# Optimization experiments

Hardware: AMD Instinct MI355X
Metric: run time of the kernel (lower is better)

Reference implementation:

```python
import jax, jax.numpy as jnp
import numpy as np

N_SEQ = 512      # n: number of generation steps (rows of x_tensor)
N_POOL = 4096    # candidate node pool size (rows of f_tensor / a_tensor)
N_FEAT = 20
E = 64           # n_node_embed
G = 128          # n_graph_embed
S = 16           # n_seq_embed
ALPHA = 20       # n_seq_alphabets


def setup_inputs() -> dict:
    key = jax.random.key(0)
    ks = jax.random.split(key, 16)
    f32 = jnp.float32

    def lin(k, fan_in, shape):
        return jax.random.normal(k, shape, f32) / jnp.sqrt(jnp.asarray(fan_in, f32))

    return {
        "x_tensor": jax.random.normal(ks[0], (N_SEQ, ALPHA), f32),
        "f_tensor": jax.random.normal(ks[1], (N_POOL, N_FEAT), f32),
        "a_tensor": jax.random.uniform(ks[2], (N_POOL, N_POOL), f32),
        "d_tensor": jax.random.uniform(ks[3], (N_POOL, N_POOL), f32),
        "w_feat": lin(ks[4], N_FEAT, (N_FEAT, E)),
        "b_feat": lin(ks[5], N_FEAT, (E,)),
        "w_gcn1": lin(ks[6], E, (E, E)),   # GCN W1, bias=False
        "w_gcn2": lin(ks[7], E, (E, E)),   # GCN W1, bias=False
        "w_graph": lin(ks[8], E, (E, G)),
        "b_graph": lin(ks[9], E, (G,)),
        "w_gate": lin(ks[10], E, (E, G)),
        "b_gate": lin(ks[11], E, (G,)),
        "w_edge": lin(ks[12], 2 * E + S + G, (2 * E + S + G, 1)),
        "b_edge": lin(ks[13], 2 * E + S + G, (1,)),
        "w_seq": lin(ks[14], ALPHA, (ALPHA, S)),
        "b_seq": lin(ks[15], ALPHA, (S,)),
    }


def reference(x_tensor, f_tensor, a_tensor, d_tensor,
              w_feat, b_feat, w_gcn1, w_gcn2,
              w_graph, b_graph, w_gate, b_gate,
              w_edge, b_edge, w_seq, b_seq):
    n = x_tensor.shape[0]
    Np = f_tensor.shape[0]
    e = w_feat.shape[1]
    g_dim = w_graph.shape[1]

    seq_embed = x_tensor @ w_seq + b_seq                 # [n, S]
    f_nodes_in = f_tensor @ w_feat + b_feat              # [Np, E]
    dAd = (d_tensor @ a_tensor) @ d_tensor               # gcn1: D A D
    h_nodes_in = (dAd @ jax.nn.relu(f_nodes_in)) @ w_gcn1  # [Np, E]

    # Chain graph at step k has k+1 nodes; A = I + sub/super diagonals.
    # Degrees: 1 (k==0), 2 at endpoints, 3 interior. Dh[k, i] = deg^{-1/2}, masked.
    ii = jnp.arange(n)
    kk = ii[:, None]
    jj = ii[None, :]
    deg = jnp.where((jj == 0) | (jj == kk), 2.0, 3.0)
    deg = jnp.where(kk == 0, 1.0, deg)
    Dh = jnp.where(jj <= kk, deg ** -0.5, 0.0).astype(x_tensor.dtype)  # [n, n]

    def step(carry, k):
        mask, idxs, h_last, h_graph = carry
        z = jnp.concatenate([
            h_nodes_in,
            jnp.broadcast_to(h_last, (Np, e)),
            jnp.broadcast_to(seq_embed[k], (Np, seq_embed.shape[1])),
            jnp.broadcast_to(h_graph, (Np, g_dim)),
        ], axis=1)                                        # [Np, 2E+S+G]
        score = ((jax.nn.relu(z) * mask[:, None]) @ w_edge)[:, 0] + b_edge[0]
        idx = jnp.argmax(score)
        mask = mask.at[idx].set(0.0)
        idxs = idxs.at[k].set(idx.astype(jnp.int32))

        # gcn2 on the chain graph over the k+1 selected nodes (band-structured).
        F_sel = f_nodes_in[idxs]                          # [n, E]; rows > k masked by dh
        dh = Dh[k]                                        # [n]
        gmat = dh[:, None] * F_sel
        g_up = jnp.pad(gmat, ((0, 1), (0, 0)))[1:]        # g[i+1]
        g_dn = jnp.pad(gmat, ((1, 0), (0, 0)))[:-1]       # g[i-1]
        dF = dh[:, None] * (gmat + g_up + g_dn)           # (D A D) F on the chain
        h_nodes = dF @ w_gcn2                             # [n, E]; rows > k are zero
        h_last_new = jnp.take(h_nodes, k, axis=0)

        valid = (jnp.arange(n) <= k).astype(h_nodes.dtype)[:, None]
        hg = h_nodes @ w_graph + b_graph
        gg = h_nodes @ w_gate + b_gate
        h_graph_new = jnp.sum(hg * jax.nn.sigmoid(gg) * valid, axis=0)
        return (mask, idxs, h_last_new, h_graph_new), score

    init = (jnp.ones(Np, x_tensor.dtype),
            jnp.zeros(n, jnp.int32),
            jnp.zeros(e, x_tensor.dtype),
            jnp.zeros(g_dim, x_tensor.dtype))
    (_, idxs, _, _), scores = jax.lax.scan(step, init, jnp.arange(n))
    return scores, idxs
```

## Files before the change

kernel.cpp:

```cpp
#include <hip/hip_runtime.h>
#include <math.h>

#define NPOOL 4096
#define NSEQ  512
#define NF    20
#define EDIM  64
#define GDIM  128
#define SDIM  16
#define ALPH  20
#define SPLITK 16
#define KSLICE (NPOOL / SPLITK)

__device__ __forceinline__ double relu_d(double x){ return x > 0.0 ? x : 0.0; }
__device__ __forceinline__ double sigm_d(double x){ return 1.0 / (1.0 + exp(-x)); }

__device__ __forceinline__ unsigned long long sortable_u64(double x) {
    x = x + 0.0;
    unsigned long long b = (unsigned long long)__double_as_longlong(x);
    return b ^ ((b >> 63) ? ~0ULL : 0x8000000000000000ULL);
}

__global__ __launch_bounds__(256) void k_prep(const float* __restrict__ f, const float* __restrict__ wf,
                       const float* __restrict__ bf, double* __restrict__ Fin, double* __restrict__ R,
                       double* __restrict__ T1z) {
    int t = blockIdx.x * 256 + threadIdx.x;
    int i = t >> 6, e = t & 63;
    double acc = (double)bf[e];
#pragma unroll
    for (int j = 0; j < NF; ++j)
        acc += (double)f[i * NF + j] * (double)wf[j * EDIM + e];
    Fin[t] = acc;
    R[t] = acc > 0.0 ? acc : 0.0;
    T1z[t] = 0.0;
}

__global__ __launch_bounds__(256) void k_seqe(const float* __restrict__ x, const float* __restrict__ wsq,
                       const float* __restrict__ bsq, double* __restrict__ seqe, int* __restrict__ rank) {
    int t = blockIdx.x * 256 + threadIdx.x;
    int k = t >> 4, s = t & 15;
    double acc = (double)bsq[s];
#pragma unroll
    for (int q = 0; q < ALPH; ++q)
        acc += (double)x[k * ALPH + q] * (double)wsq[q * SDIM + s];
    seqe[t] = acc;
    if (t < NPOOL) rank[t] = 1 << 30;
}

__global__ __launch_bounds__(256) void k_zero(double* __restrict__ buf) {
    buf[(size_t)blockIdx.x * 256 + threadIdx.x] = 0.0;
}

__global__ __launch_bounds__(256, 4) void gemm_f64_v3(const float* __restrict__ A, const double* __restrict__ B,
                                                      double* __restrict__ C) {
    __shared__ double As[32][66];
    __shared__ double Bs[32][66];
    int t  = threadIdx.x;
    int tx = t & 15;
    int ty = t >> 4;
    int row0 = blockIdx.x * 64;
    int k0   = blockIdx.y * KSLICE;
    double acc[4][4] = {};
    for (int kt = k0; kt < k0 + KSLICE; kt += 32) {
        {
            int r = t >> 2, kq = t & 3;
            const float* Ap = A + (size_t)(row0 + r) * NPOOL + kt + kq * 8;
            float4 f0 = *(const float4*)Ap;
            float4 f1 = *(const float4*)(Ap + 4);
            int kb = kq * 8;
            As[kb + 0][r] = (double)f0.x; As[kb + 1][r] = (double)f0.y;
            As[kb + 2][r] = (double)f0.z; As[kb + 3][r] = (double)f0.w;
            As[kb + 4][r] = (double)f1.x; As[kb + 5][r] = (double)f1.y;
            As[kb + 6][r] = (double)f1.z; As[kb + 7][r] = (double)f1.w;
        }
#pragma unroll
        for (int it = 0; it < 8; ++it) {
            int l = t + 256 * it;
            int kr = l >> 6, cc = l & 63;
            Bs[kr][cc] = B[(size_t)(kt + kr) * 64 + cc];
        }
        __syncthreads();
#pragma unroll
        for (int kk = 0; kk < 32; ++kk) {
            double2 a01 = *(const double2*)&As[kk][2 * ty];
            double2 a23 = *(const double2*)&As[kk][2 * ty + 32];
            double2 b01 = *(const double2*)&Bs[kk][2 * tx];
            double2 b23 = *(const double2*)&Bs[kk][2 * tx + 32];
            double a[4] = {a01.x, a01.y, a23.x, a23.y};
            double b[4] = {b01.x, b01.y, b23.x, b23.y};
#pragma unroll
            for (int i = 0; i < 4; ++i)
#pragma unroll
                for (int j = 0; j < 4; ++j)
                    acc[i][j] = fma(a[i], b[j], acc[i][j]);
        }
        __syncthreads();
    }
    int rr[4] = {2 * ty, 2 * ty + 1, 2 * ty + 32, 2 * ty + 33};
    int cc[4] = {2 * tx, 2 * tx + 1, 2 * tx + 32, 2 * tx + 33};
#pragma unroll
    for (int i = 0; i < 4; ++i)
#pragma unroll
        for (int j = 0; j < 4; ++j)
            unsafeAtomicAdd(&C[(size_t)(row0 + rr[i]) * 64 + cc[j]], acc[i][j]);
}

__global__ __launch_bounds__(256) void k_head(const double* __restrict__ T3, const float* __restrict__ w1,
                       const float* __restrict__ we, double* __restrict__ s) {
    __shared__ float w1s[64 * 64];
    int tt = threadIdx.x;
    for (int i = tt; i < 64 * 64; i += 256) w1s[i] = w1[i];
    __syncthreads();
    int row = (blockIdx.x * 256 + tt) >> 6;
    int e = tt & 63;
    const double* r = T3 + (size_t)row * 64;
    double h = 0.0;
#pragma unroll
    for (int c = 0; c < 64; ++c)
        h += r[c] * (double)w1s[c * 64 + e];
    double p = (h > 0.0 ? h : 0.0) * (double)we[e];
    for (int off = 32; off; off >>= 1) p += __shfl_down(p, off, 64);
    if (e == 0) s[row] = p;
}

__global__ __launch_bounds__(1024) void k_sort3(const double* __restrict__ s, int* __restrict__ order,
                        double* __restrict__ skey, int* __restrict__ orderB) {
    __shared__ unsigned long long P[NPOOL];
    __shared__ int idxF[NPOOL];
    __shared__ int fbS;
    int t = threadIdx.x;
    if (t == 0) fbS = 0;
    unsigned long long v[4];
#pragma unroll
    for (int i = 0; i < 4; ++i) {
        int e = 4 * t + i;
        unsigned long long srt = sortable_u64(s[e]);
        v[i] = ((~(srt >> 12)) << 12) | (unsigned long long)e;
    }

#define SHFL_ROUND(jj, kk)                                                        \
    {                                                                             \
        int lm = (int)((jj) >> 2);                                                \
        _Pragma("unroll")                                                         \
        for (int i = 0; i < 4; ++i) {                                             \
            unsigned long long p = (unsigned long long)__shfl_xor((long long)v[i], lm, 64); \
            unsigned e = 4u * (unsigned)t + (unsigned)i;                          \
            bool takeMin = (((e & (jj)) == 0u) == ((e & (kk)) == 0u));            \
            unsigned long long mn = v[i] < p ? v[i] : p;                          \
            unsigned long long mx = v[i] < p ? p : v[i];                          \
            v[i] = takeMin ? mn : mx;                                             \
        }                                                                         \
    }

#define LOCAL_ROUNDS(kk)                                                          \
    {                                                                             \
        if ((kk) >= 4) {                                                          \
            _Pragma("unroll")                                                     \
            for (int i = 0; i < 2; ++i) {                                         \
                unsigned e = 4u * (unsigned)t + (unsigned)i;                      \
                bool asc = ((e & (kk)) == 0u);                                    \
                unsigned long long a = v[i], b = v[i + 2];                        \
                bool sw = asc ? (a > b) : (a < b);                                \
                v[i] = sw ? b : a; v[i + 2] = sw ? a : b;                         \
            }                                                                     \
        }                                                                         \
        _Pragma("unroll")                                                         \
        for (int i = 0; i < 4; i += 2) {                                          \
            unsigned e = 4u * (unsigned)t + (unsigned)i;                          \
            bool asc = ((e & (kk)) == 0u);                                        \
            unsigned long long a = v[i], b = v[i + 1];                            \
            bool sw = asc ? (a > b) : (a < b);                                    \
            v[i] = sw ? b : a; v[i + 1] = sw ? a : b;                             \
        }                                                                         \
    }

    for (unsigned k = 2; k <= 256; k <<= 1) {
        for (unsigned j = k >> 1; j >= 4; j >>= 1) SHFL_ROUND(j, k)
        LOCAL_ROUNDS(k)
    }
    for (unsigned k = 512; k <= 4096; k <<= 1) {
        for (unsigned j = k >> 1; j >= 256; j >>= 1) {
            __syncthreads();
            P[4 * t + 0] = v[0]; P[4 * t + 1] = v[1];
            P[4 * t + 2] = v[2]; P[4 * t + 3] = v[3];
            __syncthreads();
            unsigned base = (4u * (unsigned)t) ^ j;
#pragma unroll
            for (int i = 0; i < 4; ++i) {
                unsigned e = 4u * (unsigned)t + (unsigned)i;
                unsigned long long p = P[base + i];
                bool takeMin = (((e & j) == 0u) == ((e & k) == 0u));
                unsigned long long mn = v[i] < p ? v[i] : p;
                unsigned long long mx = v[i] < p ? p : v[i];
                v[i] = takeMin ? mn : mx;
            }
        }
        for (unsigned j = 128; j >= 4; j >>= 1) SHFL_ROUND(j, k)
        LOCAL_ROUNDS(k)
    }
#undef SHFL_ROUND
#undef LOCAL_ROUNDS

    __syncthreads();
    P[4 * t + 0] = v[0]; P[4 * t + 1] = v[1];
    P[4 * t + 2] = v[2]; P[4 * t + 3] = v[3];
    __syncthreads();
    if (t < 512) {
        unsigned long long pa = P[t], pb = P[t + 1];
        if ((pa >> 12) == (pb >> 12)) {
            int ia = (int)(pa & 4095ULL), ib = (int)(pb & 4095ULL);
            if (sortable_u64(s[ia]) != sortable_u64(s[ib])) atomicOr(&fbS, 1);
        }
    }
    __syncthreads();
    if (fbS == 0) {
        if (t < NSEQ) {
            int id = (int)(P[t] & 4095ULL);
            order[t] = id; skey[t] = s[id]; orderB[t] = (int)(P[0] & 4095ULL);
        }
        return;
    }
    for (int i = t; i < NPOOL; i += 1024) { P[i] = sortable_u64(s[i]); idxF[i] = i; }
    __syncthreads();
    for (int k2 = 2; k2 <= NPOOL; k2 <<= 1) {
        for (int j = k2 >> 1; j > 0; j >>= 1) {
            for (int tt = t; tt < NPOOL; tt += 1024) {
                int l = tt ^ j;
                if (l > tt) {
                    unsigned long long ka = P[tt], kb = P[l];
                    int ia = idxF[tt], ib = idxF[l];
                    bool aBefore = (ka > kb) || (ka == kb && ia < ib);
                    bool asc = ((tt & k2) == 0);
                    if (asc ? !aBefore : aBefore) { P[tt] = kb; P[l] = ka; idxF[tt] = ib; idxF[l] = ia; }
                }
            }
            __syncthreads();
        }
    }
    for (int tt = t; tt < NSEQ; tt += 1024) {
        int id = idxF[tt];
        order[tt] = id; skey[tt] = s[id]; orderB[tt] = idxF[0];
    }
}

__global__ __launch_bounds__(256) void k_perk2(const double* __restrict__ Fin, const int* __restrict__ orderA,
                       const int* __restrict__ orderBv,
                       const float* __restrict__ w2, const float* __restrict__ wgr, const float* __restrict__ bgr,
                       const float* __restrict__ wga, const float* __restrict__ bga,
                       double* __restrict__ phi_inf, double* __restrict__ phi_pair, double* __restrict__ hlast) {
    const double r2 = 0.70710678118654752440;
    const double r3 = 0.57735026918962576451;
    __shared__ double u[4][64];
    __shared__ double comb[3][64];
    __shared__ double v[3][64];
    __shared__ double hgg[3][2][GDIM];
    int which = blockIdx.x >> 9;
    int k = blockIdx.x & (NSEQ - 1);
    const int* order = which ? orderBv : orderA;
    double* pi = phi_inf  + (size_t)which * NSEQ * GDIM;
    double* pp = phi_pair + (size_t)which * NSEQ * GDIM;
    double* hl = hlast    + (size_t)which * NSEQ * 64;
    int t = threadIdx.x;
    {
        int w = t >> 6, e = t & 63;
        int j = k - 3 + w;
        u[w][e] = (j >= 0) ? Fin[(size_t)order[j] * 64 + e] : 0.0;
    }
    __syncthreads();
    if (t < 192) {
        int w = t >> 6, e = t & 63;
        double dh_km3 = (k - 3 == 0) ? r2 : r3;
        double dh_km2 = (k - 2 == 0) ? r2 : r3;
        double dh_km1 = (k - 1 == 0) ? r2 : r3;
        double outer, c0, c1, c2, c3;
        if (w == 0) {
            outer = dh_km2; c0 = dh_km3; c1 = dh_km2; c2 = dh_km1; c3 = 0.0;
        } else if (w == 1) {
            outer = dh_km1; c0 = 0.0; c1 = dh_km2; c2 = dh_km1; c3 = r2;
        } else {
            if (k == 0) { outer = 1.0; c0 = c1 = c2 = 0.0; c3 = 1.0; }
            else        { outer = r2;  c0 = c1 = 0.0; c2 = dh_km1; c3 = r2; }
        }
        comb[w][e] = outer * (c0 * u[0][e] + c1 * u[1][e] + c2 * u[2][e] + c3 * u[3][e]);
    }
    __syncthreads();
    if (t < 192) {
        int w = t >> 6, e = t & 63;
        double acc = 0.0;
#pragma unroll
        for (int j = 0; j < 64; ++j)
            acc += comb[w][j] * (double)w2[j * 64 + e];
        v[w][e] = acc;
    }
    __syncthreads();
    for (int rep = 0; rep < 3; ++rep) {
        int d = t & 127, g = t >> 7;
        const float* W = g ? wga : wgr;
        const float* B = g ? bga : bgr;
        double acc = (double)B[d];
#pragma unroll
        for (int j = 0; j < 64; ++j)
            acc += v[rep][j] * (double)W[j * GDIM + d];
        hgg[rep][g][d] = acc;
    }
    __syncthreads();
    if (t < 128) {
        if (k >= 2) pi[(size_t)(k - 2) * GDIM + t] = hgg[0][0][t] * sigm_d(hgg[0][1][t]);
        double ppv = hgg[2][0][t] * sigm_d(hgg[2][1][t]);
        if (k >= 1) ppv += hgg[1][0][t] * sigm_d(hgg[1][1][t]);
        pp[(size_t)k * GDIM + t] = ppv;
    } else if (t < 192) {
        hl[(size_t)k * 64 + (t - 128)] = v[2][t - 128];
    }
}

__global__ __launch_bounds__(512) void k_scan2(const double* __restrict__ phi_inf, const double* __restrict__ phi_pair,
                       double* __restrict__ hgr) {
    __shared__ double sb[NSEQ];
    int which = blockIdx.x >> 7;
    int d = blockIdx.x & (GDIM - 1), t = threadIdx.x;
    const double* pi = phi_inf  + (size_t)which * NSEQ * GDIM;
    const double* pp = phi_pair + (size_t)which * NSEQ * GDIM;
    double* hg = hgr + (size_t)which * NSEQ * GDIM;
    sb[t] = (t >= 2) ? pi[(size_t)(t - 2) * GDIM + d] : 0.0;
    for (int off = 1; off < NSEQ; off <<= 1) {
        __syncthreads();
        double add = (t >= off) ? sb[t - off] : 0.0;
        __syncthreads();
        sb[t] += add;
    }
    __syncthreads();
    hg[(size_t)t * GDIM + d] = sb[t] + pp[(size_t)t * GDIM + d];
}

__global__ __launch_bounds__(64) void k_c2(const double* __restrict__ hlast, const double* __restrict__ hgr,
                   const double* __restrict__ seqe, const float* __restrict__ we,
                   double* __restrict__ cA, double* __restrict__ cB) {
    int which = blockIdx.x >> 9;
    int k = blockIdx.x & (NSEQ - 1), j = threadIdx.x;
    const double* hl = hlast + (size_t)which * NSEQ * 64;
    const double* hg = hgr   + (size_t)which * NSEQ * GDIM;
    double* c = which ? cB : cA;
    double ts = 0.0;
    if (k > 0) {
        ts += relu_d(hl[(size_t)(k - 1) * 64 + j]) * (double)we[64 + j];
        ts += relu_d(hg[(size_t)(k - 1) * GDIM + j]) * (double)we[144 + j];
        ts += relu_d(hg[(size_t)(k - 1) * GDIM + 64 + j]) * (double)we[208 + j];
    }
    if (j < 16) ts += relu_d(seqe[(size_t)k * SDIM + j]) * (double)we[128 + j];
    for (int off = 32; off; off >>= 1) ts += __shfl_down(ts, off, 64);
    if (j == 0) c[k] = ts;
}

__global__ __launch_bounds__(512) void k_verify2(const double* __restrict__ skey, const double* __restrict__ cA,
                         const double* __restrict__ cB, int* __restrict__ flagA, int* __restrict__ flagB) {
    __shared__ int bad;
    int t = threadIdx.x;
    if (t == 0) bad = 0;
    __syncthreads();
    if (blockIdx.x == 0) {
        if (t >= 1 && !(skey[t] + cA[t] > 0.0)) atomicOr(&bad, 1);
        __syncthreads();
        if (t == 0) flagA[0] = bad;
    } else {
        if (t >= 1 && (skey[1] + cB[t] > 0.0)) atomicOr(&bad, 1);
        __syncthreads();
        if (t == 0) flagB[0] = bad;
    }
}

__global__ __launch_bounds__(512) void k_select(const int* __restrict__ flagA, const int* __restrict__ flagB,
                        const double* __restrict__ cA, const double* __restrict__ cB,
                        const int* __restrict__ order, double* __restrict__ c,
                        int* __restrict__ idxs_sel, int* __restrict__ mode) {
    int t = threadIdx.x;
    if (flagA[0] == 0) {
        c[t] = cA[t]; idxs_sel[t] = order[t];
        if (t == 0) mode[0] = 0;
    } else if (flagB[0] == 0) {
        c[t] = cB[t]; idxs_sel[t] = order[0];
        if (t == 0) mode[0] = 1;
    } else {
        if (t == 0) mode[0] = 2;
    }
}

__global__ __launch_bounds__(256) void k_fallback(const int* __restrict__ mode,
        const double* __restrict__ Fin, const int* __restrict__ order, const double* __restrict__ skey,
        const double* __restrict__ seqe,
        const float* __restrict__ w2, const float* __restrict__ wgr, const float* __restrict__ bgr,
        const float* __restrict__ wga, const float* __restrict__ bga, const float* __restrict__ we,
        int* __restrict__ idxs_sel, double* __restrict__ c) {
    if (mode[0] != 2) return;
    const double r2 = 0.70710678118654752440;
    const double r3 = 0.57735026918962576451;
    __shared__ double u[4][64];
    __shared__ double comb[3][64];
    __shared__ double v[3][64];
    __shared__ double hgg[3][2][GDIM];
    __shared__ double Phi[GDIM], hgraph[GDIM], hlastS[64];
    __shared__ int selS, ptrS, minS_;
    int t = threadIdx.x;
    if (t < 64) { u[0][t] = u[1][t] = u[2][t] = u[3][t] = 0.0; hlastS[t] = 0.0; }
    if (t < 128) { Phi[t] = 0.0; hgraph[t] = 0.0; }
    if (t == 0) { ptrS = 0; minS_ = 0x7fffffff; }
    __syncthreads();
    for (int k = 0; k < NSEQ; ++k) {
        if (t < 64) {
            int j = t;
            double ts = relu_d(hlastS[j]) * (double)we[64 + j]
                      + relu_d(hgraph[j]) * (double)we[144 + j]
                      + relu_d(hgraph[64 + j]) * (double)we[208 + j];
            if (j < 16) ts += relu_d(seqe[(size_t)k * SDIM + j]) * (double)we[128 + j];
            for (int off = 32; off; off >>= 1) ts += __shfl_down(ts, off, 64);
            if (j == 0) {
                c[k] = ts;
                int ptr = ptrS, idx;
                if (ptr == 0) { idx = order[0]; minS_ = idx; ptrS = 1; }
                else if (skey[ptr] + ts > 0.0) {
                    idx = order[ptr];
                    if (idx < minS_) minS_ = idx;
                    ptrS = ptr + 1;
                } else idx = minS_;
                selS = idx;
                idxs_sel[k] = idx;
            }
        }
        __syncthreads();
        int idx = selS;
        if (t < 64) u[k & 3][t] = Fin[(size_t)idx * 64 + t];
        __syncthreads();
        if (t < 192) {
            int w = t >> 6, e = t & 63;
            double dh_km3 = (k - 3 == 0) ? r2 : r3;
            double dh_km2 = (k - 2 == 0) ? r2 : r3;
            double dh_km1 = (k - 1 == 0) ? r2 : r3;
            double outer, c0, c1, c2, c3;
            if (w == 0) {
                outer = dh_km2; c0 = dh_km3; c1 = dh_km2; c2 = dh_km1; c3 = 0.0;
            } else if (w == 1) {
                outer = dh_km1; c0 = 0.0; c1 = dh_km2; c2 = dh_km1; c3 = r2;
            } else {
                if (k == 0) { outer = 1.0; c0 = c1 = c2 = 0.0; c3 = 1.0; }
                else        { outer = r2;  c0 = c1 = 0.0; c2 = dh_km1; c3 = r2; }
            }
            double uu0 = u[(k - 3) & 3][e], uu1 = u[(k - 2) & 3][e], uu2 = u[(k - 1) & 3][e], uu3 = u[k & 3][e];
            comb[w][e] = outer * (c0 * uu0 + c1 * uu1 + c2 * uu2 + c3 * uu3);
        }
        __syncthreads();
        if (t < 192) {
            int w = t >> 6, e = t & 63;
            double acc = 0.0;
#pragma unroll
            for (int j = 0; j < 64; ++j)
                acc += comb[w][j] * (double)w2[j * 64 + e];
            v[w][e] = acc;
        }
        __syncthreads();
        for (int rep = 0; rep < 3; ++rep) {
            int d = t & 127, g = t >> 7;
            const float* W = g ? wga : wgr;
            const float* B = g ? bga : bgr;
            double acc = (double)B[d];
#pragma unroll
            for (int j = 0; j < 64; ++j)
                acc += v[rep][j] * (double)W[j * GDIM + d];
            hgg[rep][g][d] = acc;
        }
        __syncthreads();
        if (t < 128) {
            if (k >= 2) Phi[t] += hgg[0][0][t] * sigm_d(hgg[0][1][t]);
            double hg = Phi[t] + hgg[2][0][t] * sigm_d(hgg[2][1][t]);
            if (k >= 1) hg += hgg[1][0][t] * sigm_d(hgg[1][1][t]);
            hgraph[t] = hg;
        } else if (t < 192) {
            hlastS[t - 128] = v[2][t - 128];
        }
        __syncthreads();
    }
}

__global__ __launch_bounds__(256) void k_rank_set(const int* __restrict__ idxs_sel, int* __restrict__ rank,
                           float* __restrict__ out) {
    int t = blockIdx.x * 256 + threadIdx.x;
    if (t < NSEQ) {
        atomicMin(&rank[idxs_sel[t]], t);
        out[(size_t)NSEQ * NPOOL + t] = (float)idxs_sel[t];
    }
}

__global__ __launch_bounds__(256) void k_fill(const double* __restrict__ s, const double* __restrict__ c,
                       const int* __restrict__ rank, const float* __restrict__ be, float* __restrict__ out) {
    size_t t = (size_t)blockIdx.x * 256 + threadIdx.x;
    int k = (int)(t >> 12);
    int i = (int)(t & 4095);
    double bed = (double)be[0];
    bool masked = rank[i] < k;
    out[t] = masked ? (float)bed : (float)(s[i] + c[k] + bed);
}

extern "C" void kernel_launch(void* const* d_in, const int* in_sizes, int n_in,
                              void* d_out, int out_size, void* d_ws, size_t ws_size,
                              hipStream_t stream) {
    const float* x    = (const float*)d_in[0];
    const float* f    = (const float*)d_in[1];
    const float* amat = (const float*)d_in[2];
    const float* dmat = (const float*)d_in[3];
    const float* wf   = (const float*)d_in[4];
    const float* bf   = (const float*)d_in[5];
    const float* w1   = (const float*)d_in[6];
    const float* w2   = (const float*)d_in[7];
    const float* wgr  = (const float*)d_in[8];
    const float* bgr  = (const float*)d_in[9];
    const float* wga  = (const float*)d_in[10];
    const float* bga  = (const float*)d_in[11];
    const float* we   = (const float*)d_in[12];
    const float* be   = (const float*)d_in[13];
    const float* wsq  = (const float*)d_in[14];
    const float* bsq  = (const float*)d_in[15];
    float* out = (float*)d_out;

    char* p = (char*)d_ws;
    const size_t BIG = (size_t)NPOOL * 64 * sizeof(double);
    double* BUF0 = (double*)p; p += BIG;
    double* Fin  = (double*)p; p += BIG;
    double* BUF2 = (double*)p; p += BIG;
    double* seqe = (double*)p; p += (size_t)NSEQ * SDIM * sizeof(double);
    double* s    = (double*)p; p += (size_t)NPOOL * sizeof(double);
    double* skey = (double*)p; p += (size_t)NSEQ * sizeof(double);
    double* phi_inf  = (double*)p; p += 2 * (size_t)NSEQ * GDIM * sizeof(double);
    double* phi_pair = (double*)p; p += 2 * (size_t)NSEQ * GDIM * sizeof(double);
    double* hgr   = (double*)p; p += 2 * (size_t)NSEQ * GDIM * sizeof(double);
    double* hlast = (double*)p; p += 2 * (size_t)NSEQ * 64 * sizeof(double);
    double* cA    = (double*)p; p += (size_t)NSEQ * sizeof(double);
    double* cB    = (double*)p; p += (size_t)NSEQ * sizeof(double);
    double* c     = (double*)p; p += (size_t)NSEQ * sizeof(double);
    int* order    = (int*)p; p += 2048;
    int* orderB   = (int*)p; p += 2048;
    int* idxs_sel = (int*)p; p += 2048;
    int* rank     = (int*)p; p += (size_t)NPOOL * sizeof(int);
    int* flagA    = (int*)p; p += 256;
    int* flagB    = (int*)p; p += 256;
    int* mode     = (int*)p; p += 256;

    double* R  = BUF0;
    double* T1 = BUF2;
    double* T2 = BUF0;
    double* T3 = BUF2;

    dim3 ggrid(NPOOL / 64, SPLITK);

    k_prep<<<1024, 256, 0, stream>>>(f, wf, bf, Fin, R, T1);
    k_seqe<<<32, 256, 0, stream>>>(x, wsq, bsq, seqe, rank);

    gemm_f64_v3<<<ggrid, 256, 0, stream>>>(dmat, R, T1);
    k_zero<<<1024, 256, 0, stream>>>(T2);
    gemm_f64_v3<<<ggrid, 256, 0, stream>>>(amat, T1, T2);
    k_zero<<<1024, 256, 0, stream>>>(T3);
    gemm_f64_v3<<<ggrid, 256, 0, stream>>>(dmat, T2, T3);

    k_head<<<NPOOL / 4, 256, 0, stream>>>(T3, w1, we, s);
    k_sort3<<<1, 1024, 0, stream>>>(s, order, skey, orderB);

    k_perk2<<<2 * NSEQ, 256, 0, stream>>>(Fin, order, orderB, w2, wgr, bgr, wga, bga, phi_inf, phi_pair, hlast);
    k_scan2<<<2 * GDIM, 512, 0, stream>>>(phi_inf, phi_pair, hgr);
    k_c2<<<2 * NSEQ, 64, 0, stream>>>(hlast, hgr, seqe, we, cA, cB);
    k_verify2<<<2, 512, 0, stream>>>(skey, cA, cB, flagA, flagB);

    k_select<<<1, 512, 0, stream>>>(flagA, flagB, cA, cB, order, c, idxs_sel, mode);
    k_fallback<<<1, 256, 0, stream>>>(mode, Fin, order, skey, seqe, w2, wgr, bgr, wga, bga, we, idxs_sel, c);

    k_rank_set<<<2, 256, 0, stream>>>(idxs_sel, rank, out);
    k_fill<<<(NSEQ * NPOOL) / 256, 256, 0, stream>>>(s, c, rank, be, out);
}
```

Before: 467.3 us.

## Swizzle GEMM A-tile LDS layout, double split-K, fold buffer zeroing into prep

The f64 split-K GEMM now XOR-swizzles the row index of the transposed A tile in shared memory, to reduce LDS bank conflicts on the converted-float stores. SPLITK goes from 16 to 32, so each GEMM launches twice as many blocks over shorter K slices. The two k_zero launches are removed: separate T2 and T3 buffers are allocated and zeroed inside k_prep. In exchange the workspace grows by two 2 MB buffers and the atomic accumulation traffic into C doubles.

Result: slower. 560.8 us (+20.0%).

```diff
diff --git a/kernel.cpp b/kernel.cpp
--- a/kernel.cpp
+++ b/kernel.cpp
@@ -8,7 +8,7 @@
 #define GDIM  128
 #define SDIM  16
 #define ALPH  20
-#define SPLITK 16
+#define SPLITK 32
 #define KSLICE (NPOOL / SPLITK)
 
 __device__ __forceinline__ double relu_d(double x){ return x > 0.0 ? x : 0.0; }
@@ -22,7 +22,7 @@
 
 __global__ __launch_bounds__(256) void k_prep(const float* __restrict__ f, const float* __restrict__ wf,
                        const float* __restrict__ bf, double* __restrict__ Fin, double* __restrict__ R,
-                       double* __restrict__ T1z) {
+                       double* __restrict__ T1z, double* __restrict__ T2z, double* __restrict__ T3z) {
     int t = blockIdx.x * 256 + threadIdx.x;
     int i = t >> 6, e = t & 63;
     double acc = (double)bf[e];
@@ -31,7 +31,7 @@
         acc += (double)f[i * NF + j] * (double)wf[j * EDIM + e];
     Fin[t] = acc;
     R[t] = acc > 0.0 ? acc : 0.0;
-    T1z[t] = 0.0;
+    T1z[t] = 0.0; T2z[t] = 0.0; T3z[t] = 0.0;
 }
 
 __global__ __launch_bounds__(256) void k_seqe(const float* __restrict__ x, const float* __restrict__ wsq,
@@ -46,11 +46,7 @@
     if (t < NPOOL) rank[t] = 1 << 30;
 }
 
-__global__ __launch_bounds__(256) void k_zero(double* __restrict__ buf) {
-    buf[(size_t)blockIdx.x * 256 + threadIdx.x] = 0.0;
-}
-
-__global__ __launch_bounds__(256, 4) void gemm_f64_v3(const float* __restrict__ A, const double* __restrict__ B,
+__global__ __launch_bounds__(256, 4) void gemm_f64_v5(const float* __restrict__ A, const double* __restrict__ B,
                                                       double* __restrict__ C) {
     __shared__ double As[32][66];
     __shared__ double Bs[32][66];
@@ -67,10 +63,11 @@
             float4 f0 = *(const float4*)Ap;
             float4 f1 = *(const float4*)(Ap + 4);
             int kb = kq * 8;
-            As[kb + 0][r] = (double)f0.x; As[kb + 1][r] = (double)f0.y;
-            As[kb + 2][r] = (double)f0.z; As[kb + 3][r] = (double)f0.w;
-            As[kb + 4][r] = (double)f1.x; As[kb + 5][r] = (double)f1.y;
-            As[kb + 6][r] = (double)f1.z; As[kb + 7][r] = (double)f1.w;
+            int rs = r ^ (kq << 2);
+            As[kb + 0][rs] = (double)f0.x; As[kb + 1][rs] = (double)f0.y;
+            As[kb + 2][rs] = (double)f0.z; As[kb + 3][rs] = (double)f0.w;
+            As[kb + 4][rs] = (double)f1.x; As[kb + 5][rs] = (double)f1.y;
+            As[kb + 6][rs] = (double)f1.z; As[kb + 7][rs] = (double)f1.w;
         }
 #pragma unroll
         for (int it = 0; it < 8; ++it) {
@@ -81,8 +78,9 @@
         __syncthreads();
 #pragma unroll
         for (int kk = 0; kk < 32; ++kk) {
-            double2 a01 = *(const double2*)&As[kk][2 * ty];
-            double2 a23 = *(const double2*)&As[kk][2 * ty + 32];
+            int s = ((kk >> 3) & 3) << 2;
+            double2 a01 = *(const double2*)&As[kk][(2 * ty +  0) ^ s];
+            double2 a23 = *(const double2*)&As[kk][(2 * ty + 32) ^ s];
             double2 b01 = *(const double2*)&Bs[kk][2 * tx];
             double2 b23 = *(const double2*)&Bs[kk][2 * tx + 32];
             double a[4] = {a01.x, a01.y, a23.x, a23.y};
@@ -521,9 +519,11 @@
 
     char* p = (char*)d_ws;
     const size_t BIG = (size_t)NPOOL * 64 * sizeof(double);
-    double* BUF0 = (double*)p; p += BIG;
+    double* R    = (double*)p; p += BIG;
     double* Fin  = (double*)p; p += BIG;
-    double* BUF2 = (double*)p; p += BIG;
+    double* T1   = (double*)p; p += BIG;
+    double* T2   = (double*)p; p += BIG;
+    double* T3   = (double*)p; p += BIG;
     double* seqe = (double*)p; p += (size_t)NSEQ * SDIM * sizeof(double);
     double* s    = (double*)p; p += (size_t)NPOOL * sizeof(double);
     double* skey = (double*)p; p += (size_t)NSEQ * sizeof(double);
@@ -542,21 +542,14 @@
     int* flagB    = (int*)p; p += 256;
     int* mode     = (int*)p; p += 256;
 
-    double* R  = BUF0;
-    double* T1 = BUF2;
-    double* T2 = BUF0;
-    double* T3 = BUF2;
-
     dim3 ggrid(NPOOL / 64, SPLITK);
 
-    k_prep<<<1024, 256, 0, stream>>>(f, wf, bf, Fin, R, T1);
+    k_prep<<<1024, 256, 0, stream>>>(f, wf, bf, Fin, R, T1, T2, T3);
     k_seqe<<<32, 256, 0, stream>>>(x, wsq, bsq, seqe, rank);
 
-    gemm_f64_v3<<<ggrid, 256, 0, stream>>>(dmat, R, T1);
-    k_zero<<<1024, 256, 0, stream>>>(T2);
-    gemm_f64_v3<<<ggrid, 256, 0, stream>>>(amat, T1, T2);
-    k_zero<<<1024, 256, 0, stream>>>(T3);
-    gemm_f64_v3<<<ggrid, 256, 0, stream>>>(dmat, T2, T3);
+    gemm_f64_v5<<<ggrid, 256, 0, stream>>>(dmat, R, T1);
+    gemm_f64_v5<<<ggrid, 256, 0, stream>>>(amat, T1, T2);
+    gemm_f64_v5<<<ggrid, 256, 0, stream>>>(dmat, T2, T3);
 
     k_head<<<NPOOL / 4, 256, 0, stream>>>(T3, w1, we, s);
     k_sort3<<<1, 1024, 0, stream>>>(s, order, skey, orderB);
```
